# Kernel optimization log

Measured on AMD Instinct MI355X. Metric: run time of the kernel, lower is better.

The kernel has to match this reference:

```python
import jax, jax.numpy as jnp
import numpy as np
import math

B, H, L, D = 2, 16, 2048, 64


def setup_inputs() -> dict:
    key = jax.random.key(0)
    kq, kk, kv, km, kb = jax.random.split(key, 5)
    Q = jax.random.normal(kq, (B, H, L, D), dtype=jnp.float32)
    K = jax.random.normal(kk, (B, H, L, D), dtype=jnp.float32)
    V = jax.random.normal(kv, (B, H, L, D), dtype=jnp.float32)
    mask = jax.random.randint(km, (B, 1, L, L), 0, 2, dtype=jnp.int32)
    attn_bias = jax.random.normal(kb, (1, H, L, L), dtype=jnp.float32)
    return {"Q": Q, "K": K, "V": V, "mask": mask, "attn_bias": attn_bias,
            "last_layer_flag": 0}


def reference(Q, K, V, mask, attn_bias, last_layer_flag):
    d_tensor = K.shape[-1]
    # score: [B, H, L, L] = Q @ K^T / sqrt(d)
    score = jnp.einsum("bhqd,bhkd->bhqk", Q, K) / math.sqrt(d_tensor)
    if mask is not None:
        score = jnp.where(mask == 0, jnp.float32(-10000.0), score)
    if attn_bias is not None:
        score = score + attn_bias
    if last_layer_flag:
        return jnp.mean(score, axis=1)  # mean over heads: [B, L, L]
    score = jax.nn.softmax(score, axis=-1)
    out = jnp.einsum("bhqk,bhkd->bhqd", score, V)  # [B, H, L, D]
    return (out, score)
```

## Files before the change

### kernel.cpp

```cpp
#include <hip/hip_runtime.h>
#include <hip/hip_bf16.h>

#define Bb 2
#define Hh 16
#define Ll 2048
#define Dd 64
#define OUT_ELEMS (Bb*Hh*Ll*Dd)
#define BHL (Bb*Hh*Ll)

typedef __attribute__((ext_vector_type(8))) short bf16x8;
typedef __attribute__((ext_vector_type(4))) float f32x4;
typedef __attribute__((ext_vector_type(4))) int i32x4;

__device__ __forceinline__ unsigned int pk2(float a, float b) {
    unsigned int r;
    asm("v_cvt_pk_bf16_f32 %0, %1, %2" : "=v"(r) : "v"(a), "v"(b));
    return r;
}

__device__ __forceinline__ int swz(int row, int colByte) {
    return row * 128 + (colByte ^ ((row & 7) << 4));
}

__global__ __launch_bounds__(256)
void attn_rowsum(const float* __restrict__ Q, const float* __restrict__ K,
                 const int* __restrict__ M, const float* __restrict__ Bi,
                 float* __restrict__ ws)
{
    __shared__ char Ks[2][64 * 128];

    const int bid = blockIdx.x;
    const int ks = bid & 3;
    const int b  = (bid >> 2) & 1;
    const int qt = (bid >> 3) & 31;
    const int h  = bid >> 8;
    const int q0 = qt * 64;
    const int kbase = ks * 512;

    const int tid  = threadIdx.x;
    const int w    = tid >> 6;
    const int lane = tid & 63;
    const int g    = lane >> 4;
    const int c16  = lane & 15;
    const int qr   = w * 16 + c16;

    const float* Qp = Q + ((size_t)(b * Hh + h) * Ll + q0) * Dd;
    const float* Kp = K + (size_t)(b * Hh + h) * Ll * Dd;
    const int*   mrow = M  + (size_t)b * Ll * Ll + ((size_t)q0 + qr) * Ll;
    const float* brow = Bi + (size_t)h * Ll * Ll + ((size_t)q0 + qr) * Ll;

    bf16x8 qf[2];
    {
        const float* qrow = Qp + qr * Dd;
#pragma unroll
        for (int kk = 0; kk < 2; ++kk) {
            f32x4 a = *(const f32x4*)(qrow + kk * 32 + g * 8);
            f32x4 c = *(const f32x4*)(qrow + kk * 32 + g * 8 + 4);
            union { bf16x8 v; unsigned int u[4]; } cvt;
            cvt.u[0] = pk2(a[0], a[1]); cvt.u[1] = pk2(a[2], a[3]);
            cvt.u[2] = pk2(c[0], c[1]); cvt.u[3] = pk2(c[2], c[3]);
            qf[kk] = cvt.v;
        }
    }

    float4 kreg[4];
    i32x4  m4[4];
    f32x4  b4[4];
    const int r0 = tid >> 4, d0 = (tid & 15) * 4;

    auto issueK = [&](int k0) {
#pragma unroll
        for (int rep = 0; rep < 4; ++rep)
            kreg[rep] = *(const float4*)(Kp + (size_t)(k0 + r0 + rep * 16) * Dd + d0);
    };
    auto writeK = [&](char* buf) {
#pragma unroll
        for (int rep = 0; rep < 4; ++rep) {
            uint2 u = { pk2(kreg[rep].x, kreg[rep].y), pk2(kreg[rep].z, kreg[rep].w) };
            *(uint2*)(buf + swz(r0 + rep * 16, d0 * 2)) = u;
        }
    };
    auto issueMB = [&](int k0) {
#pragma unroll
        for (int ct = 0; ct < 4; ++ct) {
            m4[ct] = *(const i32x4*)(mrow + k0 + ct * 16 + g * 4);
            b4[ct] = *(const f32x4*)(brow + k0 + ct * 16 + g * 4);
        }
    };

    issueK(kbase);
    issueMB(kbase);
    writeK(Ks[0]);
    issueK(kbase + 64);
    __syncthreads();

    float rsv[4] = {0.f, 0.f, 0.f, 0.f};
    for (int t = 0; t < 8; ++t) {
        f32x4 sacc[4] = {{0,0,0,0},{0,0,0,0},{0,0,0,0},{0,0,0,0}};
        __builtin_amdgcn_s_setprio(1);
#pragma unroll
        for (int kk = 0; kk < 2; ++kk)
#pragma unroll
            for (int ct = 0; ct < 4; ++ct) {
                bf16x8 af = *(const bf16x8*)(Ks[t & 1] + swz(ct * 16 + c16, kk * 64 + g * 16));
                sacc[ct] = __builtin_amdgcn_mfma_f32_16x16x32_bf16(af, qf[kk], sacc[ct], 0, 0, 0);
            }
        __builtin_amdgcn_s_setprio(0);
#pragma unroll
        for (int ct = 0; ct < 4; ++ct)
#pragma unroll
            for (int r = 0; r < 4; ++r) {
                float s = m4[ct][r] == 0 ? -10000.0f
                                         : fmaf(sacc[ct][r], 0.125f, b4[ct][r]);
                rsv[ct] += __expf(s);
            }
        if (t < 7) {
            writeK(Ks[(t + 1) & 1]);
            issueMB(kbase + (t + 1) * 64);
            if (t < 6) issueK(kbase + (t + 2) * 64);
        }
        __syncthreads();
    }
    float rs = (rsv[0] + rsv[1]) + (rsv[2] + rsv[3]);
    rs += __shfl_xor(rs, 16);
    rs += __shfl_xor(rs, 32);
    if (g == 0)
        ws[(size_t)ks * BHL + (size_t)(b * Hh + h) * Ll + q0 + qr] = rs;
}

__global__ __launch_bounds__(256)
void attn_pv(const float* __restrict__ Q, const float* __restrict__ K,
             const float* __restrict__ V, const int* __restrict__ M,
             const float* __restrict__ Bi, const float* __restrict__ ws,
             float* __restrict__ out)
{
    __shared__ char Ks[2][64 * 128];
    __shared__ char VTs[64 * 128];
    __shared__ char Ps[64 * 128];

    const int bid = blockIdx.x;
    const int ks = bid & 1;
    const int b  = (bid >> 1) & 1;
    const int qt = (bid >> 2) & 31;
    const int h  = bid >> 7;
    const int q0 = qt * 64;
    const int kbase = ks * 1024;
    const int NTB = 16;

    const int tid  = threadIdx.x;
    const int w    = tid >> 6;
    const int lane = tid & 63;
    const int g    = lane >> 4;
    const int c16  = lane & 15;
    const int qr   = w * 16 + c16;

    const float* Qp = Q + ((size_t)(b * Hh + h) * Ll + q0) * Dd;
    const float* Kp = K + (size_t)(b * Hh + h) * Ll * Dd;
    const float* Vp = V + (size_t)(b * Hh + h) * Ll * Dd;
    float* Op = out + ((size_t)(b * Hh + h) * Ll + q0) * Dd;
    const int*   mrow = M  + (size_t)b * Ll * Ll + ((size_t)q0 + qr) * Ll;
    const float* brow = Bi + (size_t)h * Ll * Ll + ((size_t)q0 + qr) * Ll;
    float*       srow = out + OUT_ELEMS + ((size_t)(b * Hh + h) * Ll + q0 + qr) * Ll;

    float inv;
    {
        size_t idx = (size_t)(b * Hh + h) * Ll + q0 + qr;
        float s = ws[idx] + ws[(size_t)BHL + idx] + ws[2 * (size_t)BHL + idx]
                + ws[3 * (size_t)BHL + idx];
        inv = 1.0f / s;
    }

    bf16x8 qf[2];
    {
        const float* qrow = Qp + qr * Dd;
#pragma unroll
        for (int kk = 0; kk < 2; ++kk) {
            f32x4 a = *(const f32x4*)(qrow + kk * 32 + g * 8);
            f32x4 c = *(const f32x4*)(qrow + kk * 32 + g * 8 + 4);
            union { bf16x8 v; unsigned int u[4]; } cvt;
            cvt.u[0] = pk2(a[0], a[1]); cvt.u[1] = pk2(a[2], a[3]);
            cvt.u[2] = pk2(c[0], c[1]); cvt.u[3] = pk2(c[2], c[3]);
            qf[kk] = cvt.v;
        }
    }

    float4 kreg[4];
    float  vreg[16];
    i32x4  m4[4];
    f32x4  b4[4];
    const int r0 = tid >> 4, d0 = (tid & 15) * 4;

    auto issueK = [&](int k0) {
#pragma unroll
        for (int rep = 0; rep < 4; ++rep)
            kreg[rep] = *(const float4*)(Kp + (size_t)(k0 + r0 + rep * 16) * Dd + d0);
    };
    auto writeK = [&](char* buf) {
#pragma unroll
        for (int rep = 0; rep < 4; ++rep) {
            uint2 u = { pk2(kreg[rep].x, kreg[rep].y), pk2(kreg[rep].z, kreg[rep].w) };
            *(uint2*)(buf + swz(r0 + rep * 16, d0 * 2)) = u;
        }
    };
    auto issueV = [&](int k0) {
#pragma unroll
        for (int r = 0; r < 4; ++r)
#pragma unroll
            for (int i = 0; i < 4; ++i)
                vreg[r * 4 + i] = Vp[(size_t)(k0 + w * 16 + r * 4 + i) * Dd + lane];
    };
    auto writeV = [&]() {
#pragma unroll
        for (int r = 0; r < 4; ++r) {
            uint2 u = { pk2(vreg[r * 4 + 0], vreg[r * 4 + 1]),
                        pk2(vreg[r * 4 + 2], vreg[r * 4 + 3]) };
            *(uint2*)(VTs + swz(lane, (w * 16 + r * 4) * 2)) = u;
        }
    };
    auto issueMB = [&](int k0) {
#pragma unroll
        for (int ct = 0; ct < 4; ++ct) {
            m4[ct] = *(const i32x4*)(mrow + k0 + ct * 16 + g * 4);
            b4[ct] = *(const f32x4*)(brow + k0 + ct * 16 + g * 4);
        }
    };

    issueK(kbase);
    issueMB(kbase);
    issueV(kbase);
    writeK(Ks[0]);
    issueK(kbase + 64);

    f32x4 oacc[4] = {{0,0,0,0},{0,0,0,0},{0,0,0,0},{0,0,0,0}};
    for (int t = 0; t < NTB; ++t) {
        const int k0 = kbase + t * 64;
        __syncthreads();
        writeV();
        if (t + 1 < NTB) {
            writeK(Ks[(t + 1) & 1]);
            issueV(k0 + 64);
            if (t + 2 < NTB) issueK(k0 + 128);
        }
        f32x4 sacc[4] = {{0,0,0,0},{0,0,0,0},{0,0,0,0},{0,0,0,0}};
        __builtin_amdgcn_s_setprio(1);
#pragma unroll
        for (int kk = 0; kk < 2; ++kk)
#pragma unroll
            for (int ct = 0; ct < 4; ++ct) {
                bf16x8 af = *(const bf16x8*)(Ks[t & 1] + swz(ct * 16 + c16, kk * 64 + g * 16));
                sacc[ct] = __builtin_amdgcn_mfma_f32_16x16x32_bf16(af, qf[kk], sacc[ct], 0, 0, 0);
            }
        __builtin_amdgcn_s_setprio(0);
#pragma unroll
        for (int ct = 0; ct < 4; ++ct) {
            f32x4 p;
#pragma unroll
            for (int r = 0; r < 4; ++r) {
                float s = m4[ct][r] == 0 ? -10000.0f
                                         : fmaf(sacc[ct][r], 0.125f, b4[ct][r]);
                p[r] = __expf(s) * inv;
            }
            __builtin_nontemporal_store(p, (f32x4*)(srow + k0 + ct * 16 + g * 4));
            uint2 u = { pk2(p[0], p[1]), pk2(p[2], p[3]) };
            *(uint2*)(Ps + swz(qr, ct * 32 + g * 8)) = u;
        }
        if (t + 1 < NTB) issueMB(k0 + 64);
        __syncthreads();
        __builtin_amdgcn_s_setprio(1);
#pragma unroll
        for (int kk = 0; kk < 2; ++kk) {
            bf16x8 pf = *(const bf16x8*)(Ps + swz(qr, kk * 64 + g * 16));
#pragma unroll
            for (int dt = 0; dt < 4; ++dt) {
                bf16x8 vf = *(const bf16x8*)(VTs + swz(dt * 16 + c16, kk * 64 + g * 16));
                oacc[dt] = __builtin_amdgcn_mfma_f32_16x16x32_bf16(pf, vf, oacc[dt], 0, 0, 0);
            }
        }
        __builtin_amdgcn_s_setprio(0);
    }

#pragma unroll
    for (int dt = 0; dt < 4; ++dt)
#pragma unroll
        for (int r = 0; r < 4; ++r)
            unsafeAtomicAdd(&Op[(w * 16 + g * 4 + r) * Dd + dt * 16 + c16], oacc[dt][r]);
}

extern "C" void kernel_launch(void* const* d_in, const int* in_sizes, int n_in,
                              void* d_out, int out_size, void* d_ws, size_t ws_size,
                              hipStream_t stream) {
    const float* Q  = (const float*)d_in[0];
    const float* K  = (const float*)d_in[1];
    const float* V  = (const float*)d_in[2];
    const int*   M  = (const int*)d_in[3];
    const float* Bi = (const float*)d_in[4];
    float* out = (float*)d_out;
    float* ws  = (float*)d_ws;

    hipMemsetAsync(out, 0, (size_t)OUT_ELEMS * sizeof(float), stream);

    attn_rowsum<<<dim3(4096), dim3(256), 0, stream>>>(Q, K, M, Bi, ws);
    attn_pv    <<<dim3(2048), dim3(256), 0, stream>>>(Q, K, V, M, Bi, ws, out);
}
```

Before: 511.7 us.

## Store unnormalized bf16 exp scores in workspace and add fused fallback kernel

The first pass now writes the unnormalized exp(score) values as bf16 into a large workspace alongside the row sums. The second pass only reads those bf16 values and V, normalizes them into the fp32 score output, and applies 1/rowsum to the PV accumulator, so it no longer rereads mask and bias or recomputes QK^T. If the workspace is too small, a single fused kernel per query tile runs two passes over K instead. This trades the second mask/bias read for a bf16 workspace write and read, and the exported probabilities are rounded through bf16, which loosens precision.

After: 461.3 us. 9.9% less time.

```diff
diff --git a/kernel.cpp b/kernel.cpp
--- a/kernel.cpp
+++ b/kernel.cpp
@@ -7,6 +7,7 @@
 #define Dd 64
 #define OUT_ELEMS (Bb*Hh*Ll*Dd)
 #define BHL (Bb*Hh*Ll)
+#define NT (Ll/64)
 
 typedef __attribute__((ext_vector_type(8))) short bf16x8;
 typedef __attribute__((ext_vector_type(4))) float f32x4;
@@ -17,17 +18,26 @@
     asm("v_cvt_pk_bf16_f32 %0, %1, %2" : "=v"(r) : "v"(a), "v"(b));
     return r;
 }
-
+__device__ __forceinline__ float bf2f(short s) {
+    union { float f; unsigned u; } c;
+    c.u = ((unsigned)(unsigned short)s) << 16;
+    return c.f;
+}
+__device__ __forceinline__ void bar() {
+    asm volatile("s_waitcnt lgkmcnt(0)" ::: "memory");
+    __builtin_amdgcn_s_barrier();
+}
 __device__ __forceinline__ int swz(int row, int colByte) {
     return row * 128 + (colByte ^ ((row & 7) << 4));
 }
 
 __global__ __launch_bounds__(256)
-void attn_rowsum(const float* __restrict__ Q, const float* __restrict__ K,
-                 const int* __restrict__ M, const float* __restrict__ Bi,
-                 float* __restrict__ ws)
+void attn_exp(const float* __restrict__ Q, const float* __restrict__ K,
+              const int* __restrict__ M, const float* __restrict__ Bi,
+              float* __restrict__ ws)
 {
     __shared__ char Ks[2][64 * 128];
+    __shared__ char Ps[64 * 128];
 
     const int bid = blockIdx.x;
     const int ks = bid & 3;
@@ -35,7 +45,7 @@
     const int qt = (bid >> 3) & 31;
     const int h  = bid >> 8;
     const int q0 = qt * 64;
-    const int kbase = ks * 512;
+    const int kb = ks * 512;
 
     const int tid  = threadIdx.x;
     const int w    = tid >> 6;
@@ -48,6 +58,8 @@
     const float* Kp = K + (size_t)(b * Hh + h) * Ll * Dd;
     const int*   mrow = M  + (size_t)b * Ll * Ll + ((size_t)q0 + qr) * Ll;
     const float* brow = Bi + (size_t)h * Ll * Ll + ((size_t)q0 + qr) * Ll;
+    unsigned short* srow = (unsigned short*)(ws + 4 * (size_t)BHL)
+                         + ((size_t)(b * Hh + h) * Ll + q0 + qr) * (size_t)Ll;
 
     bf16x8 qf[2];
     {
@@ -88,11 +100,11 @@
         }
     };
 
-    issueK(kbase);
-    issueMB(kbase);
+    issueK(kb);
+    issueMB(kb);
     writeK(Ks[0]);
-    issueK(kbase + 64);
-    __syncthreads();
+    issueK(kb + 64);
+    bar();
 
     float rsv[4] = {0.f, 0.f, 0.f, 0.f};
     for (int t = 0; t < 8; ++t) {
@@ -107,19 +119,28 @@
             }
         __builtin_amdgcn_s_setprio(0);
 #pragma unroll
-        for (int ct = 0; ct < 4; ++ct)
+        for (int ct = 0; ct < 4; ++ct) {
+            f32x4 e;
 #pragma unroll
             for (int r = 0; r < 4; ++r) {
                 float s = m4[ct][r] == 0 ? -10000.0f
                                          : fmaf(sacc[ct][r], 0.125f, b4[ct][r]);
-                rsv[ct] += __expf(s);
-            }
-        if (t < 7) {
-            writeK(Ks[(t + 1) & 1]);
-            issueMB(kbase + (t + 1) * 64);
-            if (t < 6) issueK(kbase + (t + 2) * 64);
-        }
-        __syncthreads();
+                e[r] = __expf(s);
+                rsv[ct] += e[r];
+            }
+            uint2 u = { pk2(e[0], e[1]), pk2(e[2], e[3]) };
+            *(uint2*)(Ps + swz(qr, ct * 32 + g * 8)) = u;
+        }
+        const int kc = kb + t * 64;
+#pragma unroll
+        for (int half = 0; half < 2; ++half) {
+            bf16x8 d = *(const bf16x8*)(Ps + swz(qr, half * 64 + g * 16));
+            *(bf16x8*)(srow + kc + half * 32 + g * 8) = d;
+        }
+        writeK(Ks[(t + 1) & 1]);
+        issueK(kb + ((t + 2) & 7) * 64);
+        issueMB(kb + ((t + 1) & 7) * 64);
+        bar();
     }
     float rs = (rsv[0] + rsv[1]) + (rsv[2] + rsv[3]);
     rs += __shfl_xor(rs, 16);
@@ -129,14 +150,10 @@
 }
 
 __global__ __launch_bounds__(256)
-void attn_pv(const float* __restrict__ Q, const float* __restrict__ K,
-             const float* __restrict__ V, const int* __restrict__ M,
-             const float* __restrict__ Bi, const float* __restrict__ ws,
-             float* __restrict__ out)
+void attn_pv2(const float* __restrict__ V, const float* __restrict__ ws,
+              float* __restrict__ out)
 {
-    __shared__ char Ks[2][64 * 128];
-    __shared__ char VTs[64 * 128];
-    __shared__ char Ps[64 * 128];
+    __shared__ char VTs[2][64 * 128];
 
     const int bid = blockIdx.x;
     const int ks = bid & 1;
@@ -144,8 +161,7 @@
     const int qt = (bid >> 2) & 31;
     const int h  = bid >> 7;
     const int q0 = qt * 64;
-    const int kbase = ks * 1024;
-    const int NTB = 16;
+    const int kb = ks * 1024;
 
     const int tid  = threadIdx.x;
     const int w    = tid >> 6;
@@ -154,21 +170,116 @@
     const int c16  = lane & 15;
     const int qr   = w * 16 + c16;
 
-    const float* Qp = Q + ((size_t)(b * Hh + h) * Ll + q0) * Dd;
-    const float* Kp = K + (size_t)(b * Hh + h) * Ll * Dd;
     const float* Vp = V + (size_t)(b * Hh + h) * Ll * Dd;
     float* Op = out + ((size_t)(b * Hh + h) * Ll + q0) * Dd;
-    const int*   mrow = M  + (size_t)b * Ll * Ll + ((size_t)q0 + qr) * Ll;
-    const float* brow = Bi + (size_t)h * Ll * Ll + ((size_t)q0 + qr) * Ll;
-    float*       srow = out + OUT_ELEMS + ((size_t)(b * Hh + h) * Ll + q0 + qr) * Ll;
-
-    float inv;
+    float* prow = out + OUT_ELEMS + ((size_t)(b * Hh + h) * Ll + q0 + qr) * (size_t)Ll;
+    const unsigned short* srow = (const unsigned short*)(ws + 4 * (size_t)BHL)
+                               + ((size_t)(b * Hh + h) * Ll + q0 + qr) * (size_t)Ll;
+
+    float inv, invO[4];
     {
         size_t idx = (size_t)(b * Hh + h) * Ll + q0 + qr;
         float s = ws[idx] + ws[(size_t)BHL + idx] + ws[2 * (size_t)BHL + idx]
                 + ws[3 * (size_t)BHL + idx];
         inv = 1.0f / s;
-    }
+#pragma unroll
+        for (int r = 0; r < 4; ++r) invO[r] = __shfl(inv, g * 4 + r);
+    }
+
+    float vreg[16];
+    auto issueV = [&](int k0) {
+#pragma unroll
+        for (int r = 0; r < 4; ++r)
+#pragma unroll
+            for (int i = 0; i < 4; ++i)
+                vreg[r * 4 + i] = Vp[(size_t)(k0 + w * 16 + r * 4 + i) * Dd + lane];
+    };
+    auto writeV = [&](char* buf) {
+#pragma unroll
+        for (int r = 0; r < 4; ++r) {
+            uint2 u = { pk2(vreg[r * 4 + 0], vreg[r * 4 + 1]),
+                        pk2(vreg[r * 4 + 2], vreg[r * 4 + 3]) };
+            *(uint2*)(buf + swz(lane, (w * 16 + r * 4) * 2)) = u;
+        }
+    };
+
+    bf16x8 pa[2];
+    auto loadA = [&](int t) {
+        pa[0] = *(const bf16x8*)(srow + kb + t * 64 + g * 8);
+        pa[1] = *(const bf16x8*)(srow + kb + t * 64 + 32 + g * 8);
+    };
+
+    issueV(kb);
+    loadA(0);
+    writeV(VTs[0]);
+    issueV(kb + 64);
+    bar();
+
+    f32x4 oacc[4] = {{0,0,0,0},{0,0,0,0},{0,0,0,0},{0,0,0,0}};
+    for (int t = 0; t < 16; ++t) {
+        __builtin_amdgcn_s_setprio(1);
+#pragma unroll
+        for (int kk = 0; kk < 2; ++kk)
+#pragma unroll
+            for (int dt = 0; dt < 4; ++dt) {
+                bf16x8 vf = *(const bf16x8*)(VTs[t & 1] + swz(dt * 16 + c16, kk * 64 + g * 16));
+                oacc[dt] = __builtin_amdgcn_mfma_f32_16x16x32_bf16(pa[kk], vf, oacc[dt], 0, 0, 0);
+            }
+        __builtin_amdgcn_s_setprio(0);
+        const int k0 = kb + t * 64;
+#pragma unroll
+        for (int kk = 0; kk < 2; ++kk) {
+            f32x4 p0, p1;
+#pragma unroll
+            for (int j = 0; j < 4; ++j) {
+                p0[j] = bf2f(pa[kk][j]) * inv;
+                p1[j] = bf2f(pa[kk][4 + j]) * inv;
+            }
+            __builtin_nontemporal_store(p0, (f32x4*)(prow + k0 + kk * 32 + g * 8));
+            __builtin_nontemporal_store(p1, (f32x4*)(prow + k0 + kk * 32 + g * 8 + 4));
+        }
+        loadA((t + 1) & 15);
+        writeV(VTs[(t + 1) & 1]);
+        issueV(kb + ((t + 2) & 15) * 64);
+        bar();
+    }
+#pragma unroll
+    for (int dt = 0; dt < 4; ++dt)
+#pragma unroll
+        for (int r = 0; r < 4; ++r)
+            unsafeAtomicAdd(&Op[(w * 16 + g * 4 + r) * Dd + dt * 16 + c16],
+                            oacc[dt][r] * invO[r]);
+}
+
+__global__ __launch_bounds__(256)
+void attn_fused(const float* __restrict__ Q, const float* __restrict__ K,
+                const float* __restrict__ V, const int* __restrict__ M,
+                const float* __restrict__ Bi, float* __restrict__ out)
+{
+    __shared__ char Ks[2][64 * 128];
+    __shared__ char VTs[2][64 * 128];
+    __shared__ char Ps[64 * 128];
+
+    const int bid = blockIdx.x;
+    const int b  = bid & 1;
+    const int qt = (bid >> 1) & 31;
+    const int h  = bid >> 6;
+    const int q0 = qt * 64;
+
+    const int tid  = threadIdx.x;
+    const int w    = tid >> 6;
+    const int lane = tid & 63;
+    const int g    = lane >> 4;
+    const int c16  = lane & 15;
+    const int qr   = w * 16 + c16;
+
+    const float* Qp = Q  + ((size_t)(b * Hh + h) * Ll + q0) * Dd;
+    const float* Kp = K  + (size_t)(b * Hh + h) * Ll * Dd;
+    const float* Vp = V  + (size_t)(b * Hh + h) * Ll * Dd;
+    float* Op = out + ((size_t)(b * Hh + h) * Ll + q0) * Dd;
+    const int*   mrow = M  + (size_t)b * Ll * Ll + ((size_t)q0 + qr) * Ll;
+    const float* brow = Bi + (size_t)h * Ll * Ll + ((size_t)q0 + qr) * Ll;
+    float*       srow = out + OUT_ELEMS + ((size_t)(b * Hh + h) * Ll + q0 + qr) * Ll;
 
     bf16x8 qf[2];
     {
@@ -209,12 +320,12 @@
             for (int i = 0; i < 4; ++i)
                 vreg[r * 4 + i] = Vp[(size_t)(k0 + w * 16 + r * 4 + i) * Dd + lane];
     };
-    auto writeV = [&]() {
+    auto writeV = [&](char* buf) {
 #pragma unroll
         for (int r = 0; r < 4; ++r) {
             uint2 u = { pk2(vreg[r * 4 + 0], vreg[r * 4 + 1]),
                         pk2(vreg[r * 4 + 2], vreg[r * 4 + 3]) };
-            *(uint2*)(VTs + swz(lane, (w * 16 + r * 4) * 2)) = u;
+            *(uint2*)(buf + swz(lane, (w * 16 + r * 4) * 2)) = u;
         }
     };
     auto issueMB = [&](int k0) {
@@ -224,33 +335,55 @@
             b4[ct] = *(const f32x4*)(brow + k0 + ct * 16 + g * 4);
         }
     };
-
-    issueK(kbase);
-    issueMB(kbase);
-    issueV(kbase);
+    auto mfmaST = [&](const char* kbuf, f32x4 (&sacc)[4]) {
+        __builtin_amdgcn_s_setprio(1);
+#pragma unroll
+        for (int kk = 0; kk < 2; ++kk)
+#pragma unroll
+            for (int ct = 0; ct < 4; ++ct) {
+                bf16x8 af = *(const bf16x8*)(kbuf + swz(ct * 16 + c16, kk * 64 + g * 16));
+                sacc[ct] = __builtin_amdgcn_mfma_f32_16x16x32_bf16(af, qf[kk], sacc[ct], 0, 0, 0);
+            }
+        __builtin_amdgcn_s_setprio(0);
+    };
+
+    issueK(0);
+    issueMB(0);
     writeK(Ks[0]);
-    issueK(kbase + 64);
+    issueK(64);
+    bar();
+    float rsv[4] = {0.f, 0.f, 0.f, 0.f};
+    for (int t = 0; t < NT; ++t) {
+        f32x4 sacc[4] = {{0,0,0,0},{0,0,0,0},{0,0,0,0},{0,0,0,0}};
+        mfmaST(Ks[t & 1], sacc);
+#pragma unroll
+        for (int ct = 0; ct < 4; ++ct)
+#pragma unroll
+            for (int r = 0; r < 4; ++r) {
+                float s = m4[ct][r] == 0 ? -10000.0f
+                                         : fmaf(sacc[ct][r], 0.125f, b4[ct][r]);
+                rsv[ct] += __expf(s);
+            }
+        writeK(Ks[(t + 1) & 1]);
+        issueK(((t + 2) & (NT - 1)) * 64);
+        issueMB(((t + 1) & (NT - 1)) * 64);
+        bar();
+    }
+    float rs = (rsv[0] + rsv[1]) + (rsv[2] + rsv[3]);
+    rs += __shfl_xor(rs, 16);
+    rs += __shfl_xor(rs, 32);
+    const float inv = 1.0f / rs;
+
+    issueV(0);
+    writeV(VTs[0]);
+    issueV(64);
+    bar();
 
     f32x4 oacc[4] = {{0,0,0,0},{0,0,0,0},{0,0,0,0},{0,0,0,0}};
-    for (int t = 0; t < NTB; ++t) {
-        const int k0 = kbase + t * 64;
-        __syncthreads();
-        writeV();
-        if (t + 1 < NTB) {
-            writeK(Ks[(t + 1) & 1]);
-            issueV(k0 + 64);
-            if (t + 2 < NTB) issueK(k0 + 128);
-        }
+    for (int t = 0; t < NT; ++t) {
         f32x4 sacc[4] = {{0,0,0,0},{0,0,0,0},{0,0,0,0},{0,0,0,0}};
-        __builtin_amdgcn_s_setprio(1);
-#pragma unroll
-        for (int kk = 0; kk < 2; ++kk)
-#pragma unroll
-            for (int ct = 0; ct < 4; ++ct) {
-                bf16x8 af = *(const bf16x8*)(Ks[t & 1] + swz(ct * 16 + c16, kk * 64 + g * 16));
-                sacc[ct] = __builtin_amdgcn_mfma_f32_16x16x32_bf16(af, qf[kk], sacc[ct], 0, 0, 0);
-            }
-        __builtin_amdgcn_s_setprio(0);
+        mfmaST(Ks[t & 1], sacc);
+        const int k0 = t * 64;
 #pragma unroll
         for (int ct = 0; ct < 4; ++ct) {
             f32x4 p;
@@ -264,26 +397,33 @@
             uint2 u = { pk2(p[0], p[1]), pk2(p[2], p[3]) };
             *(uint2*)(Ps + swz(qr, ct * 32 + g * 8)) = u;
         }
-        if (t + 1 < NTB) issueMB(k0 + 64);
-        __syncthreads();
         __builtin_amdgcn_s_setprio(1);
 #pragma unroll
         for (int kk = 0; kk < 2; ++kk) {
             bf16x8 pf = *(const bf16x8*)(Ps + swz(qr, kk * 64 + g * 16));
 #pragma unroll
             for (int dt = 0; dt < 4; ++dt) {
-                bf16x8 vf = *(const bf16x8*)(VTs + swz(dt * 16 + c16, kk * 64 + g * 16));
+                bf16x8 vf = *(const bf16x8*)(VTs[t & 1] + swz(dt * 16 + c16, kk * 64 + g * 16));
                 oacc[dt] = __builtin_amdgcn_mfma_f32_16x16x32_bf16(pf, vf, oacc[dt], 0, 0, 0);
             }
         }
         __builtin_amdgcn_s_setprio(0);
-    }
-
+        if (t + 1 < NT) {
+            writeK(Ks[(t + 1) & 1]);
+            writeV(VTs[(t + 1) & 1]);
+            issueMB((t + 1) * 64);
+        }
+        if (t + 2 < NT) {
+            issueK((t + 2) * 64);
+            issueV((t + 2) * 64);
+        }
+        bar();
+    }
 #pragma unroll
     for (int dt = 0; dt < 4; ++dt)
 #pragma unroll
         for (int r = 0; r < 4; ++r)
-            unsafeAtomicAdd(&Op[(w * 16 + g * 4 + r) * Dd + dt * 16 + c16], oacc[dt][r]);
+            Op[(w * 16 + g * 4 + r) * Dd + dt * 16 + c16] = oacc[dt][r];
 }
 
 extern "C" void kernel_launch(void* const* d_in, const int* in_sizes, int n_in,
@@ -297,8 +437,13 @@
     float* out = (float*)d_out;
     float* ws  = (float*)d_ws;
 
-    hipMemsetAsync(out, 0, (size_t)OUT_ELEMS * sizeof(float), stream);
-
-    attn_rowsum<<<dim3(4096), dim3(256), 0, stream>>>(Q, K, M, Bi, ws);
-    attn_pv    <<<dim3(2048), dim3(256), 0, stream>>>(Q, K, V, M, Bi, ws, out);
-}
+    const size_t need = 4ull * BHL * sizeof(float)
+                      + (size_t)BHL * Ll * sizeof(unsigned short);
+    if (ws_size >= need) {
+        hipMemsetAsync(out, 0, (size_t)OUT_ELEMS * sizeof(float), stream);
+        attn_exp<<<dim3(4096), dim3(256), 0, stream>>>(Q, K, M, Bi, ws);
+        attn_pv2<<<dim3(2048), dim3(256), 0, stream>>>(V, ws, out);
+    } else {
+        attn_fused<<<dim3(Bb * Hh * (Ll / 64)), dim3(256), 0, stream>>>(Q, K, V, M, Bi, out);
+    }
+}
```
